# Performance work log

Hardware: AMD Instinct MI355X
Metric: run time of the kernel (lower is better)

The kernel has to match this reference:

```python
import jax, jax.numpy as jnp
import numpy as np

NEG = -1.0e9  # matches the -1000000000.0 masking constant in the torch source


def setup_inputs() -> dict:
    key = jax.random.key(0)
    k1, k2, k3, k4 = jax.random.split(key, 4)
    B, N, M, D = 32, 2048, 512, 128
    sequence1 = jax.random.normal(k1, (B, N, D), dtype=jnp.float32)
    sequence2 = jax.random.normal(k2, (B, M, D), dtype=jnp.float32)
    sequence1_mask = jax.random.randint(k3, (B, N), 0, 2, dtype=jnp.int32)
    sequence2_mask = jax.random.randint(k4, (B, M), 0, 2, dtype=jnp.int32)
    return {
        "sequence1": sequence1,
        "sequence2": sequence2,
        "sequence1_mask": sequence1_mask,
        "sequence2_mask": sequence2_mask,
    }


def reference(sequence1, sequence2, sequence1_mask, sequence2_mask):
    # sequence1: [B, n, d] (context), sequence2: [B, m, d] (question)
    dt = sequence1.dtype
    m1 = sequence1_mask.astype(dt)  # [B, n]
    m2 = sequence2_mask.astype(dt)  # [B, m]

    # DotProduct similarity over the (virtually) tiled tensors -> [B, n, m].
    # Fused: no [B,n,m,d] intermediates.
    S = jnp.einsum('bnd,bmd->bnm', sequence1, sequence2)

    # masked softmax over sequence2 positions (context-to-question attention)
    a2 = jax.nn.softmax(S + (1.0 - m2)[:, None, :] * NEG, axis=-1)  # [B, n, m]
    seq1_seq2_attention = jnp.einsum('bnm,bmd->bnd', a2, sequence2)

    # one-shot question-to-context attention: masked max over m, softmax over n
    s1 = jnp.max(S * m2[:, None, :] + (1.0 - m2)[:, None, :] * NEG, axis=-1)  # [B, n]
    a1 = jax.nn.softmax(s1 + (1.0 - m1) * NEG, axis=-1)  # [B, n]
    seq2_seq1_attention = jnp.einsum('bn,bnd->bd', a1, sequence1)  # [B, d]

    return (seq1_seq2_attention, a2, seq2_seq1_attention, a1)
```

## Files before the change

### kernel.cpp

```cpp
#include <hip/hip_runtime.h>
#include <stdint.h>

#define NEGC (-1.0e9f)

typedef __attribute__((ext_vector_type(8))) short bf16x8;
typedef __attribute__((ext_vector_type(4))) float f32x4;

__device__ __align__(16) unsigned short g_S2H[32u * 512u * 128u];
__device__ __align__(16) unsigned short g_S2L[32u * 512u * 128u];
__device__ __align__(16) unsigned short g_VT[32u * 128u * 512u];
__device__ float g_part[32 * 8 * 128];

__device__ __forceinline__ unsigned short f2bf(float f) {
    union { float f; unsigned int u; } v; v.f = f;
    unsigned int r = v.u + 0x7fffu + ((v.u >> 16) & 1u);
    return (unsigned short)(r >> 16);
}
__device__ __forceinline__ float bf2f(unsigned short h) {
    union { float f; unsigned int u; } v; v.u = ((unsigned int)h) << 16;
    return v.f;
}

__device__ __forceinline__ void gl_lds16(const void* g, void* l) {
    __builtin_amdgcn_global_load_lds(
        (const __attribute__((address_space(1))) unsigned int*)g,
        (__attribute__((address_space(3))) unsigned int*)l, 16, 0, 0);
}

__global__ __launch_bounds__(256) void k_prep(const float* __restrict__ seq2) {
    const int b = blockIdx.x >> 1, h = blockIdx.x & 1, t = threadIdx.x;
    const float4* src = (const float4*)(seq2 + (size_t)(b * 512 + h * 256) * 128);
    ushort4* dh = (ushort4*)(g_S2H + (size_t)(b * 512 + h * 256) * 128);
    ushort4* dl = (ushort4*)(g_S2L + (size_t)(b * 512 + h * 256) * 128);
#pragma unroll 4
    for (int p = 0; p < 32; ++p) {
        float4 v = src[p * 256 + t];
        float vs[4] = {v.x, v.y, v.z, v.w};
        unsigned short hh[4], ll[4];
#pragma unroll
        for (int i = 0; i < 4; ++i) { hh[i] = f2bf(vs[i]); ll[i] = f2bf(vs[i] - bf2f(hh[i])); }
        ushort4 uh{hh[0], hh[1], hh[2], hh[3]};
        ushort4 ul{ll[0], ll[1], ll[2], ll[3]};
        dh[p * 256 + t] = uh;
        dl[p * 256 + t] = ul;
    }
    const int d = h * 64 + (t & 63), mq = t >> 6;
#pragma unroll 2
    for (int j = 0; j < 16; ++j) {
        int mb = (mq * 16 + j) * 8;
        unsigned short pk[8];
#pragma unroll
        for (int i = 0; i < 8; ++i)
            pk[i] = f2bf(seq2[(size_t)(b * 512 + mb + i) * 128 + d]);
        ushort4 p0{pk[0], pk[1], pk[2], pk[3]};
        ushort4 p1{pk[4], pk[5], pk[6], pk[7]};
        *(ushort4*)(g_VT + (size_t)(b * 128 + d) * 512 + mb) = p0;
        *(ushort4*)(g_VT + (size_t)(b * 128 + d) * 512 + mb + 4) = p1;
    }
}

#define KBASE 16384
#define TBASE 32768
#define M2OFF 49152
#define REDOFF 49664
#define LDS_TOTAL 50176

__global__ __launch_bounds__(256, 3) void bidir_main(
    const float* __restrict__ seq1,
    const int* __restrict__ m1, const int* __restrict__ m2,
    float* __restrict__ out0, float* __restrict__ a2out,
    float* __restrict__ a1log)
{
    __shared__ __align__(16) char smem[LDS_TOTAL];

    const int t = threadIdx.x, lane = t & 63, w = t >> 6;
    const int wr = w >> 1, wc = w & 1, q = lane >> 4, fr = lane & 15;
    const int orig = blockIdx.x;
    const int swzb = (orig & 7) * 256 + (orig >> 3);
    const int b = swzb >> 6, n0 = (swzb & 63) << 5;

    unsigned char* M2u8 = (unsigned char*)(smem + M2OFF);
    float* REDm = (float*)(smem + REDOFF);
    float* REDs = (float*)(smem + REDOFF + 256);

    if (t < 128) {
        int4 v = ((const int4*)(m2 + b * 512))[t];
        uchar4 u{(unsigned char)v.x, (unsigned char)v.y, (unsigned char)v.z, (unsigned char)v.w};
        *(uchar4*)(M2u8 + t * 4) = u;
    }
    {
        const float4* s1p = (const float4*)(seq1 + (size_t)(b * 2048 + n0) * 128);
#pragma unroll
        for (int p = 0; p < 4; ++p) {
            int idx = p * 256 + t;
            int row = idx >> 5, c4 = idx & 31;
            float4 v = s1p[idx];
            float vs[4] = {v.x, v.y, v.z, v.w};
            unsigned short hh[4], ll[4];
#pragma unroll
            for (int i = 0; i < 4; ++i) { hh[i] = f2bf(vs[i]); ll[i] = f2bf(vs[i] - bf2f(hh[i])); }
            ushort4 uh{hh[0], hh[1], hh[2], hh[3]};
            ushort4 ul{ll[0], ll[1], ll[2], ll[3]};
            int off = (row * 256 + c4 * 8) ^ ((row & 7) << 4);
            *(ushort4*)(smem + off) = uh;
            *(ushort4*)(smem + 8192 + off) = ul;
        }
    }
    __syncthreads();

    bf16x8 ah[4], al[4];
    {
        int row = wr * 16 + fr;
        int sw = (row & 7) << 4;
#pragma unroll
        for (int ks = 0; ks < 4; ++ks) {
            int off = (row * 256 + ks * 64 + q * 16) ^ sw;
            ah[ks] = *(const bf16x8*)(smem + off);
            al[ks] = *(const bf16x8*)(smem + 8192 + off);
        }
    }

    f32x4 acc[8][2];
#pragma unroll
    for (int i = 0; i < 8; ++i) {
        acc[i][0] = (f32x4){0.f, 0.f, 0.f, 0.f};
        acc[i][1] = (f32x4){0.f, 0.f, 0.f, 0.f};
    }

#pragma unroll
    for (int mt = 0; mt < 8; ++mt) {
        {
            const unsigned short* sb = (w < 2) ? g_S2H : g_S2L;
            const char* srcb = (const char*)(sb + (size_t)(b * 512 + (w & 1) * 256 + mt * 32) * 128);
            char* dstb = smem + KBASE + w * 8192;
#pragma unroll
            for (int i = 0; i < 8; ++i) {
                int r = i * 4 + q;
                int so = r * 256 + ((fr * 16) ^ ((r & 7) << 4));
                gl_lds16(srcb + so, dstb + i * 1024);
            }
        }
        __syncthreads();
        {
            const char* KH = smem + KBASE + wc * 8192;
            const char* KL = smem + KBASE + 16384 + wc * 8192;
#pragma unroll
            for (int s = 0; s < 2; ++s) {
                int rrow = s * 16 + fr;
                int sw = (fr & 7) << 4;
#pragma unroll
                for (int ks = 0; ks < 4; ++ks) {
                    int off = (rrow * 256 + ks * 64 + q * 16) ^ sw;
                    bf16x8 bh = *(const bf16x8*)(KH + off);
                    bf16x8 bl = *(const bf16x8*)(KL + off);
                    acc[mt][s] = __builtin_amdgcn_mfma_f32_16x16x32_bf16(al[ks], bh, acc[mt][s], 0, 0, 0);
                    acc[mt][s] = __builtin_amdgcn_mfma_f32_16x16x32_bf16(ah[ks], bl, acc[mt][s], 0, 0, 0);
                    acc[mt][s] = __builtin_amdgcn_mfma_f32_16x16x32_bf16(ah[ks], bh, acc[mt][s], 0, 0, 0);
                }
            }
        }
        __syncthreads();
    }

#pragma unroll
    for (int mt = 0; mt < 8; ++mt)
#pragma unroll
        for (int s = 0; s < 2; ++s) {
            int m = wc * 256 + mt * 32 + s * 16 + fr;
            bool keep = M2u8[m] != 0;
#pragma unroll
            for (int r = 0; r < 4; ++r)
                acc[mt][s][r] = keep ? acc[mt][s][r] : NEGC;
        }
    float rmax[4];
#pragma unroll
    for (int r = 0; r < 4; ++r) rmax[r] = NEGC;
#pragma unroll
    for (int mt = 0; mt < 8; ++mt)
#pragma unroll
        for (int s = 0; s < 2; ++s)
#pragma unroll
            for (int r = 0; r < 4; ++r) rmax[r] = fmaxf(rmax[r], acc[mt][s][r]);
#pragma unroll
    for (int off = 1; off < 16; off <<= 1)
#pragma unroll
        for (int r = 0; r < 4; ++r) rmax[r] = fmaxf(rmax[r], __shfl_xor(rmax[r], off));
    if (fr == 0) {
#pragma unroll
        for (int r = 0; r < 4; ++r) REDm[wc * 32 + wr * 16 + q * 4 + r] = rmax[r];
    }
    __syncthreads();
    float RM[4];
#pragma unroll
    for (int r = 0; r < 4; ++r) {
        int rl = wr * 16 + q * 4 + r;
        RM[r] = fmaxf(REDm[rl], REDm[32 + rl]);
    }
    if (t < 32) {
        float v = fmaxf(REDm[t], REDm[32 + t]);
        float m1v = (float)m1[b * 2048 + n0 + t];
        a1log[b * 2048 + n0 + t] = v + (1.0f - m1v) * NEGC;
    }
    float rs[4] = {0.f, 0.f, 0.f, 0.f};
#pragma unroll
    for (int mt = 0; mt < 8; ++mt)
#pragma unroll
        for (int s = 0; s < 2; ++s)
#pragma unroll
            for (int r = 0; r < 4; ++r) {
                float e = __expf(acc[mt][s][r] - RM[r]);
                acc[mt][s][r] = e;
                rs[r] += e;
            }
#pragma unroll
    for (int off = 1; off < 16; off <<= 1)
#pragma unroll
        for (int r = 0; r < 4; ++r) rs[r] += __shfl_xor(rs[r], off);
    if (fr == 0) {
#pragma unroll
        for (int r = 0; r < 4; ++r) REDs[wc * 32 + wr * 16 + q * 4 + r] = rs[r];
    }
    __syncthreads();
    float rinv[4];
#pragma unroll
    for (int r = 0; r < 4; ++r) {
        int rl = wr * 16 + q * 4 + r;
        rinv[r] = 1.0f / (REDs[rl] + REDs[32 + rl]);
    }
#pragma unroll
    for (int mt = 0; mt < 8; ++mt)
#pragma unroll
        for (int s = 0; s < 2; ++s) {
            int m = wc * 256 + mt * 32 + s * 16 + fr;
#pragma unroll
            for (int r = 0; r < 4; ++r) {
                int rl = wr * 16 + q * 4 + r;
                float v = acc[mt][s][r] * rinv[r];
                a2out[(size_t)(b * 2048 + n0 + rl) * 512 + m] = v;
                int off = (rl * 1024 + m * 2) ^ ((rl & 7) << 4);
                *(unsigned short*)(smem + off) = f2bf(v);
            }
        }

    f32x4 oacc[4];
#pragma unroll
    for (int c = 0; c < 4; ++c) oacc[c] = (f32x4){0.f, 0.f, 0.f, 0.f};

#pragma unroll
    for (int mt = 0; mt < 8; ++mt) {
        {
            char* dstb = smem + TBASE + w * 4096;
#pragma unroll
            for (int i = 0; i < 4; ++i) {
                int d = w * 32 + i * 8 + (lane >> 3);
                int cb = (lane & 7) * 16;
                size_t so = (size_t)(b * 128 + d) * 1024 + mt * 128 + (cb ^ ((d & 7) << 4));
                gl_lds16((const char*)g_VT + so, dstb + i * 1024);
            }
        }
        __syncthreads();
        {
            int arow = wr * 16 + fr;
            int asw = (fr & 7) << 4;
#pragma unroll
            for (int ks = 0; ks < 2; ++ks) {
                int aoff = (arow * 1024 + mt * 128 + ks * 64 + q * 16) ^ asw;
                bf16x8 pa = *(const bf16x8*)(smem + aoff);
#pragma unroll
                for (int c = 0; c < 4; ++c) {
                    int d = wc * 64 + c * 16 + fr;
                    int boff = (d * 128 + ks * 64 + q * 16) ^ ((d & 7) << 4);
                    bf16x8 bv = *(const bf16x8*)(smem + TBASE + boff);
                    oacc[c] = __builtin_amdgcn_mfma_f32_16x16x32_bf16(pa, bv, oacc[c], 0, 0, 0);
                }
            }
        }
        __syncthreads();
    }

#pragma unroll
    for (int c = 0; c < 4; ++c)
#pragma unroll
        for (int r = 0; r < 4; ++r) {
            int rl = wr * 16 + q * 4 + r;
            int d = wc * 64 + c * 16 + fr;
            out0[(size_t)(b * 2048 + n0 + rl) * 128 + d] = oacc[c][r];
        }
}

__global__ __launch_bounds__(256) void k_a1(float* __restrict__ a1slot) {
    __shared__ float wred[4];
    const int b = blockIdx.x, t = threadIdx.x, lane = t & 63, w = t >> 6;

    const float4* Lp = (const float4*)(a1slot + (size_t)b * 2048);
    float4 La = Lp[t * 2], Lb = Lp[t * 2 + 1];
    float l[8] = {La.x, La.y, La.z, La.w, Lb.x, Lb.y, Lb.z, Lb.w};

    float lmax = l[0];
#pragma unroll
    for (int j = 1; j < 8; ++j) lmax = fmaxf(lmax, l[j]);
#pragma unroll
    for (int off = 1; off < 64; off <<= 1) lmax = fmaxf(lmax, __shfl_xor(lmax, off));
    if (lane == 0) wred[w] = lmax;
    __syncthreads();
    float bmax = fmaxf(fmaxf(wred[0], wred[1]), fmaxf(wred[2], wred[3]));

    float e[8]; float s = 0.f;
#pragma unroll
    for (int j = 0; j < 8; ++j) { e[j] = __expf(l[j] - bmax); s += e[j]; }
#pragma unroll
    for (int off = 1; off < 64; off <<= 1) s += __shfl_xor(s, off);
    __syncthreads();
    if (lane == 0) wred[w] = s;
    __syncthreads();
    float inv = 1.0f / (wred[0] + wred[1] + wred[2] + wred[3]);

    float4 o1{e[0] * inv, e[1] * inv, e[2] * inv, e[3] * inv};
    float4 o2v{e[4] * inv, e[5] * inv, e[6] * inv, e[7] * inv};
    ((float4*)(a1slot + (size_t)b * 2048))[t * 2] = o1;
    ((float4*)(a1slot + (size_t)b * 2048))[t * 2 + 1] = o2v;
}

__global__ __launch_bounds__(256) void k_gemv(const float* __restrict__ seq1,
                                              const float* __restrict__ a1) {
    __shared__ float a1b[256];
    __shared__ float4 red[8][32];
    const int bid = blockIdx.x, b = bid >> 3, ch = bid & 7, t = threadIdx.x;
    const int n0 = ch * 256;
    if (t < 64) ((float4*)a1b)[t] = ((const float4*)(a1 + (size_t)b * 2048 + n0))[t];
    __syncthreads();
    const int d4 = t & 31, sl = t >> 5;
    float4 acc{0.f, 0.f, 0.f, 0.f};
    const float4* s1 = (const float4*)(seq1 + (size_t)(b * 2048 + n0 + sl * 32) * 128);
#pragma unroll 8
    for (int j = 0; j < 32; ++j) {
        float wv = a1b[sl * 32 + j];
        float4 v = s1[j * 32 + d4];
        acc.x += wv * v.x; acc.y += wv * v.y; acc.z += wv * v.z; acc.w += wv * v.w;
    }
    red[sl][d4] = acc;
    __syncthreads();
    if (t < 32) {
        float4 s0 = red[0][t];
#pragma unroll
        for (int c = 1; c < 8; ++c) {
            float4 v = red[c][t];
            s0.x += v.x; s0.y += v.y; s0.z += v.z; s0.w += v.w;
        }
        ((float4*)(g_part + (size_t)(b * 8 + ch) * 128))[t] = s0;
    }
}

__global__ __launch_bounds__(128) void k_final(float* __restrict__ out2) {
    const int b = blockIdx.x, t = threadIdx.x;
    float s = 0.f;
#pragma unroll
    for (int c = 0; c < 8; ++c) s += g_part[(size_t)(b * 8 + c) * 128 + t];
    out2[b * 128 + t] = s;
}

extern "C" void kernel_launch(void* const* d_in, const int* in_sizes, int n_in,
                              void* d_out, int out_size, void* d_ws, size_t ws_size,
                              hipStream_t stream) {
    const float* seq1 = (const float*)d_in[0];
    const float* seq2 = (const float*)d_in[1];
    const int*   m1   = (const int*)d_in[2];
    const int*   m2   = (const int*)d_in[3];
    (void)d_ws; (void)ws_size; (void)n_in; (void)in_sizes;

    float* out  = (float*)d_out;
    float* out0 = out;
    float* a2o  = out + 8388608;
    float* o2   = out + 41943040;
    float* a1o  = out + 41947136;

    k_prep<<<dim3(64), dim3(256), 0, stream>>>(seq2);
    bidir_main<<<dim3(2048), dim3(256), 0, stream>>>(seq1, m1, m2, out0, a2o, a1o);
    k_a1<<<dim3(32), dim3(256), 0, stream>>>(a1o);
    k_gemv<<<dim3(256), dim3(256), 0, stream>>>(seq1, a1o);
    k_final<<<dim3(32), dim3(128), 0, stream>>>(o2);
}
```

Before: 95.09 us.

## Parallelize prep transpose, hoist first tile loads, nontemporal stores, drop final kernel

k_prep now runs 512 blocks instead of 64 and builds the V transpose through an LDS tile, replacing the strided global reads. In bidir_main, the first K tile and the first V^T tile are issued before the preceding setup work (mask load, softmax normalization), so those loads overlap with it. The a2 and out0 stores become nontemporal, keeping the large output stream from displacing cached data. The k_final reduction kernel is removed: k_a1 zeros out2 and k_gemv accumulates into it with atomicAdd, which makes the float sum order nondeterministic.

```diff
diff --git a/kernel.cpp b/kernel.cpp
--- a/kernel.cpp
+++ b/kernel.cpp
@@ -9,7 +9,6 @@
 __device__ __align__(16) unsigned short g_S2H[32u * 512u * 128u];
 __device__ __align__(16) unsigned short g_S2L[32u * 512u * 128u];
 __device__ __align__(16) unsigned short g_VT[32u * 128u * 512u];
-__device__ float g_part[32 * 8 * 128];
 
 __device__ __forceinline__ unsigned short f2bf(float f) {
     union { float f; unsigned int u; } v; v.f = f;
@@ -28,35 +27,38 @@
 }
 
 __global__ __launch_bounds__(256) void k_prep(const float* __restrict__ seq2) {
-    const int b = blockIdx.x >> 1, h = blockIdx.x & 1, t = threadIdx.x;
-    const float4* src = (const float4*)(seq2 + (size_t)(b * 512 + h * 256) * 128);
-    ushort4* dh = (ushort4*)(g_S2H + (size_t)(b * 512 + h * 256) * 128);
-    ushort4* dl = (ushort4*)(g_S2L + (size_t)(b * 512 + h * 256) * 128);
-#pragma unroll 4
-    for (int p = 0; p < 32; ++p) {
-        float4 v = src[p * 256 + t];
+    __shared__ unsigned short Lh[32 * 130];
+    const int b = blockIdx.x >> 4, c = blockIdx.x & 15, t = threadIdx.x;
+    const int m0 = c * 32;
+
+    const float4* src = (const float4*)(seq2 + (size_t)(b * 512 + m0) * 128);
+    ushort4* dh = (ushort4*)(g_S2H + (size_t)(b * 512 + m0) * 128);
+    ushort4* dl = (ushort4*)(g_S2L + (size_t)(b * 512 + m0) * 128);
+#pragma unroll
+    for (int p = 0; p < 4; ++p) {
+        int idx = p * 256 + t;
+        int row = idx >> 5, c4 = idx & 31;
+        float4 v = src[idx];
         float vs[4] = {v.x, v.y, v.z, v.w};
         unsigned short hh[4], ll[4];
 #pragma unroll
         for (int i = 0; i < 4; ++i) { hh[i] = f2bf(vs[i]); ll[i] = f2bf(vs[i] - bf2f(hh[i])); }
         ushort4 uh{hh[0], hh[1], hh[2], hh[3]};
         ushort4 ul{ll[0], ll[1], ll[2], ll[3]};
-        dh[p * 256 + t] = uh;
-        dl[p * 256 + t] = ul;
-    }
-    const int d = h * 64 + (t & 63), mq = t >> 6;
-#pragma unroll 2
-    for (int j = 0; j < 16; ++j) {
-        int mb = (mq * 16 + j) * 8;
-        unsigned short pk[8];
-#pragma unroll
-        for (int i = 0; i < 8; ++i)
-            pk[i] = f2bf(seq2[(size_t)(b * 512 + mb + i) * 128 + d]);
-        ushort4 p0{pk[0], pk[1], pk[2], pk[3]};
-        ushort4 p1{pk[4], pk[5], pk[6], pk[7]};
-        *(ushort4*)(g_VT + (size_t)(b * 128 + d) * 512 + mb) = p0;
-        *(ushort4*)(g_VT + (size_t)(b * 128 + d) * 512 + mb + 4) = p1;
-    }
+        dh[idx] = uh;
+        dl[idx] = ul;
+#pragma unroll
+        for (int i = 0; i < 4; ++i) Lh[row * 130 + c4 * 4 + i] = hh[i];
+    }
+    __syncthreads();
+
+    const int d = t >> 1, sub = t & 1;
+    unsigned short pk[16];
+#pragma unroll
+    for (int j = 0; j < 16; ++j) pk[j] = Lh[(sub * 16 + j) * 130 + d];
+    unsigned short* dst = g_VT + (size_t)(b * 128 + d) * 512 + m0 + sub * 16;
+    *(bf16x8*)dst = *(bf16x8*)pk;
+    *(bf16x8*)(dst + 8) = *(bf16x8*)(pk + 8);
 }
 
 #define KBASE 16384
@@ -83,6 +85,18 @@
     float* REDm = (float*)(smem + REDOFF);
     float* REDs = (float*)(smem + REDOFF + 256);
 
+    {
+        const unsigned short* sb = (w < 2) ? g_S2H : g_S2L;
+        const char* srcb = (const char*)(sb + (size_t)(b * 512 + (w & 1) * 256) * 128);
+        char* dstb = smem + KBASE + w * 8192;
+#pragma unroll
+        for (int i = 0; i < 8; ++i) {
+            int r = i * 4 + q;
+            int so = r * 256 + ((fr * 16) ^ ((r & 7) << 4));
+            gl_lds16(srcb + so, dstb + i * 1024);
+        }
+    }
+
     if (t < 128) {
         int4 v = ((const int4*)(m2 + b * 512))[t];
         uchar4 u{(unsigned char)v.x, (unsigned char)v.y, (unsigned char)v.z, (unsigned char)v.w};
@@ -129,7 +143,7 @@
 
 #pragma unroll
     for (int mt = 0; mt < 8; ++mt) {
-        {
+        if (mt > 0) {
             const unsigned short* sb = (w < 2) ? g_S2H : g_S2L;
             const char* srcb = (const char*)(sb + (size_t)(b * 512 + (w & 1) * 256 + mt * 32) * 128);
             char* dstb = smem + KBASE + w * 8192;
@@ -227,6 +241,18 @@
         int rl = wr * 16 + q * 4 + r;
         rinv[r] = 1.0f / (REDs[rl] + REDs[32 + rl]);
     }
+
+    {
+        char* dstb = smem + TBASE + w * 4096;
+#pragma unroll
+        for (int i = 0; i < 4; ++i) {
+            int d = w * 32 + i * 8 + (lane >> 3);
+            int cb = (lane & 7) * 16;
+            size_t so = (size_t)(b * 128 + d) * 1024 + (cb ^ ((d & 7) << 4));
+            gl_lds16((const char*)g_VT + so, dstb + i * 1024);
+        }
+    }
+
 #pragma unroll
     for (int mt = 0; mt < 8; ++mt)
 #pragma unroll
@@ -236,7 +262,7 @@
             for (int r = 0; r < 4; ++r) {
                 int rl = wr * 16 + q * 4 + r;
                 float v = acc[mt][s][r] * rinv[r];
-                a2out[(size_t)(b * 2048 + n0 + rl) * 512 + m] = v;
+                __builtin_nontemporal_store(v, &a2out[(size_t)(b * 2048 + n0 + rl) * 512 + m]);
                 int off = (rl * 1024 + m * 2) ^ ((rl & 7) << 4);
                 *(unsigned short*)(smem + off) = f2bf(v);
             }
@@ -248,7 +274,7 @@
 
 #pragma unroll
     for (int mt = 0; mt < 8; ++mt) {
-        {
+        if (mt > 0) {
             char* dstb = smem + TBASE + w * 4096;
 #pragma unroll
             for (int i = 0; i < 4; ++i) {
@@ -284,13 +310,16 @@
         for (int r = 0; r < 4; ++r) {
             int rl = wr * 16 + q * 4 + r;
             int d = wc * 64 + c * 16 + fr;
-            out0[(size_t)(b * 2048 + n0 + rl) * 128 + d] = oacc[c][r];
-        }
-}
-
-__global__ __launch_bounds__(256) void k_a1(float* __restrict__ a1slot) {
+            __builtin_nontemporal_store(oacc[c][r], &out0[(size_t)(b * 2048 + n0 + rl) * 128 + d]);
+        }
+}
+
+__global__ __launch_bounds__(256) void k_a1(float* __restrict__ a1slot,
+                                            float* __restrict__ out2) {
     __shared__ float wred[4];
     const int b = blockIdx.x, t = threadIdx.x, lane = t & 63, w = t >> 6;
+
+    if (t < 128) out2[b * 128 + t] = 0.f;
 
     const float4* Lp = (const float4*)(a1slot + (size_t)b * 2048);
     float4 La = Lp[t * 2], Lb = Lp[t * 2 + 1];
@@ -322,7 +351,8 @@
 }
 
 __global__ __launch_bounds__(256) void k_gemv(const float* __restrict__ seq1,
-                                              const float* __restrict__ a1) {
+                                              const float* __restrict__ a1,
+                                              float* __restrict__ out2) {
     __shared__ float a1b[256];
     __shared__ float4 red[8][32];
     const int bid = blockIdx.x, b = bid >> 3, ch = bid & 7, t = threadIdx.x;
@@ -347,16 +377,12 @@
             float4 v = red[c][t];
             s0.x += v.x; s0.y += v.y; s0.z += v.z; s0.w += v.w;
         }
-        ((float4*)(g_part + (size_t)(b * 8 + ch) * 128))[t] = s0;
-    }
-}
-
-__global__ __launch_bounds__(128) void k_final(float* __restrict__ out2) {
-    const int b = blockIdx.x, t = threadIdx.x;
-    float s = 0.f;
-#pragma unroll
-    for (int c = 0; c < 8; ++c) s += g_part[(size_t)(b * 8 + c) * 128 + t];
-    out2[b * 128 + t] = s;
+        float* dst = out2 + b * 128 + t * 4;
+        atomicAdd(dst + 0, s0.x);
+        atomicAdd(dst + 1, s0.y);
+        atomicAdd(dst + 2, s0.z);
+        atomicAdd(dst + 3, s0.w);
+    }
 }
 
 extern "C" void kernel_launch(void* const* d_in, const int* in_sizes, int n_in,
@@ -374,9 +400,8 @@
     float* o2   = out + 41943040;
     float* a1o  = out + 41947136;
 
-    k_prep<<<dim3(64), dim3(256), 0, stream>>>(seq2);
+    k_prep<<<dim3(512), dim3(256), 0, stream>>>(seq2);
     bidir_main<<<dim3(2048), dim3(256), 0, stream>>>(seq1, m1, m2, out0, a2o, a1o);
-    k_a1<<<dim3(32), dim3(256), 0, stream>>>(a1o);
-    k_gemv<<<dim3(256), dim3(256), 0, stream>>>(seq1, a1o);
-    k_final<<<dim3(32), dim3(128), 0, stream>>>(o2);
-}
+    k_a1<<<dim3(32), dim3(256), 0, stream>>>(a1o, o2);
+    k_gemv<<<dim3(256), dim3(256), 0, stream>>>(seq1, a1o, o2);
+}
```

Result: no change. 95.84 us (+0.8%).
